# Optimization experiments

Measured on AMD Instinct MI355X. Metric: run time of the kernel, lower is better.

The kernel has to match this reference:

```python
import jax, jax.numpy as jnp
import numpy as np

HIDDEN = 64
PRED_LEN = 12
B = 32768
OBS_LEN = 20


def setup_inputs() -> dict:
    key = jax.random.key(0)
    ks = jax.random.split(key, 16)
    bound = 1.0 / np.sqrt(HIDDEN)  # PyTorch default LSTM init range
    u = lambda k, shape: jax.random.uniform(k, shape, jnp.float32, -bound, bound)
    return {
        "obs_seq": jax.random.normal(ks[0], (B, OBS_LEN, 2), jnp.float32),
        "w_ih_l0": u(ks[1], (4 * HIDDEN, 2)),
        "w_hh_l0": u(ks[2], (4 * HIDDEN, HIDDEN)),
        "b_ih_l0": u(ks[3], (4 * HIDDEN,)),
        "b_hh_l0": u(ks[4], (4 * HIDDEN,)),
        "w_ih_l1": u(ks[5], (4 * HIDDEN, HIDDEN)),
        "w_hh_l1": u(ks[6], (4 * HIDDEN, HIDDEN)),
        "b_ih_l1": u(ks[7], (4 * HIDDEN,)),
        "b_hh_l1": u(ks[8], (4 * HIDDEN,)),
        "dec_w_ih": u(ks[9], (4 * HIDDEN, 2)),
        "dec_w_hh": u(ks[10], (4 * HIDDEN, HIDDEN)),
        "dec_b_ih": u(ks[11], (4 * HIDDEN,)),
        "dec_b_hh": u(ks[12], (4 * HIDDEN,)),
        "out_w": u(ks[13], (2, HIDDEN)),
        "out_b": u(ks[14], (2,)),
    }


def _lstm_cell(x, h, c, w_ih, w_hh, b):
    # PyTorch gate order: input, forget, cell(g), output
    z = x @ w_ih.T + h @ w_hh.T + b
    i, f, g, o = jnp.split(z, 4, axis=-1)
    c_new = jax.nn.sigmoid(f) * c + jax.nn.sigmoid(i) * jnp.tanh(g)
    h_new = jax.nn.sigmoid(o) * jnp.tanh(c_new)
    return h_new, c_new


def _lstm_layer(x_tbd, w_ih, w_hh, b, h0, c0):
    # x_tbd: (T, B, in). Returns all hidden states (T, B, H) and final (h, c).
    def step(carry, x_t):
        h, c = carry
        h, c = _lstm_cell(x_t, h, c, w_ih, w_hh, b)
        return (h, c), h
    (h, c), hs = jax.lax.scan(step, (h0, c0), x_tbd)
    return hs, h, c


def reference(obs_seq, w_ih_l0, w_hh_l0, b_ih_l0, b_hh_l0,
              w_ih_l1, w_hh_l1, b_ih_l1, b_hh_l1,
              dec_w_ih, dec_w_hh, dec_b_ih, dec_b_hh, out_w, out_b):
    # Eval-mode reference: dropout layers act as identity.
    bsz = obs_seq.shape[0]
    x = jnp.transpose(obs_seq, (1, 0, 2))  # (T, B, 2)
    zeros = jnp.zeros((bsz, HIDDEN), obs_seq.dtype)
    hs1, _, _ = _lstm_layer(x, w_ih_l0, w_hh_l0, b_ih_l0 + b_hh_l0, zeros, zeros)
    _, h, c = _lstm_layer(hs1, w_ih_l1, w_hh_l1, b_ih_l1 + b_hh_l1, zeros, zeros)
    db = dec_b_ih + dec_b_hh

    def dec_step(carry, _):
        h, c, xin = carry
        h, c = _lstm_cell(xin, h, c, dec_w_ih, dec_w_hh, db)
        out = h @ out_w.T + out_b
        return (h, c, out), out

    _, preds = jax.lax.scan(dec_step, (h, c, obs_seq[:, -1, :]), None, length=PRED_LEN)
    return jnp.transpose(preds, (1, 0, 2))  # (B, pred_len, 2)
```

## Files before the change

### kernel.cpp

```cpp
#include <hip/hip_runtime.h>
#include <math.h>

#define BATCH 32768
#define TOBS  20
#define TPRED 12

typedef _Float16 f16;
typedef f16  half8 __attribute__((ext_vector_type(8)));
typedef float f32x4 __attribute__((ext_vector_type(4)));

#define LOG2E 1.44269504088896f
#define K2    2.88539008177793f

#define OFF_W0A  0u
#define OFF_WDA  36864u
#define OFF_W1   73728u
#define OFF_B1   139264u
#define OFF_OUT  140288u
#define WS_NEED  ((size_t)143360)

__device__ __forceinline__ float frcp(float x){
#if __has_builtin(__builtin_amdgcn_rcpf)
  return __builtin_amdgcn_rcpf(x);
#else
  return 1.0f/x;
#endif
}
__device__ __forceinline__ float fexp2(float x){
#if __has_builtin(__builtin_amdgcn_exp2f)
  return __builtin_amdgcn_exp2f(x);
#else
  return exp2f(x);
#endif
}
__device__ __forceinline__ f32x4 MFMA(half8 a, half8 b, f32x4 c){
  return __builtin_amdgcn_mfma_f32_16x16x32_f16(a, b, c, 0, 0, 0);
}
__device__ __forceinline__ int grow(int rt, int m){
  return (m&3)*64 + (m>>2)*16 + rt;
}
__device__ __forceinline__ float gsc(int m){
  return ((m&3)==2) ? (2.0f*LOG2E) : LOG2E;
}

__device__ __forceinline__ float gate_h(const f32x4 a, float& c){
  const float ei = fexp2(-a[0]);
  const float ef = fexp2(-a[1]);
  const float eg = fexp2(-a[2]);
  const float eo = fexp2(-a[3]);
  const float fg  = frcp(1.0f + ef);
  const float rig = frcp((1.0f + ei)*(1.0f + eg));
  const float cn  = fg*c + (1.0f - eg)*rig;
  c = cn;
  const float ec = fexp2(cn * -K2);
  return (1.0f - ec) * frcp((1.0f + eo)*(1.0f + ec));
}

__global__ void prep_pack(const float* __restrict__ wih0, const float* __restrict__ whh0,
                          const float* __restrict__ bih0, const float* __restrict__ bhh0,
                          const float* __restrict__ wih1, const float* __restrict__ whh1,
                          const float* __restrict__ bih1, const float* __restrict__ bhh1,
                          const float* __restrict__ dwih, const float* __restrict__ dwhh,
                          const float* __restrict__ dbih, const float* __restrict__ dbhh,
                          const float* __restrict__ outw, const float* __restrict__ outb,
                          char* __restrict__ ws)
{
  const int tid = blockIdx.x*blockDim.x + threadIdx.x;
  const int stride = gridDim.x*blockDim.x;

  f16* w0 = (f16*)(ws + OFF_W0A);
  f16* wd = (f16*)(ws + OFF_WDA);
  for (int idx = tid; idx < 16384; idx += stride) {
    int i = idx & 7, lane = (idx>>3)&63, kt = (idx>>9)&1, rt = idx>>10;
    int m = lane&15;
    int row = grow(rt, m);
    int k   = kt*32 + (lane>>4)*8 + i;
    float s = gsc(m);
    w0[idx] = (f16)(whh0[row*64 + k]*s);
    wd[idx] = (f16)(dwhh[row*64 + k]*s);
  }
  for (int idx = tid; idx < 2048; idx += stride) {
    int i = idx & 7, m = (idx>>3)&15, rt = idx>>7;
    int row = grow(rt, m);
    float s = gsc(m);
    float v0 = (i==0) ? wih0[row*2] : (i==1) ? wih0[row*2+1] : (i==2) ? (bih0[row]+bhh0[row]) : 0.f;
    float vd = (i==0) ? dwih[row*2] : (i==1) ? dwih[row*2+1] : (i==2) ? (dbih[row]+dbhh[row]) : 0.f;
    w0[16384 + idx] = (f16)(v0*s);
    wd[16384 + idx] = (f16)(vd*s);
  }
  f16* w1 = (f16*)(ws + OFF_W1);
  for (int idx = tid; idx < 32768; idx += stride) {
    int i = idx & 7, lane = (idx>>3)&63, kt = (idx>>9)&3, rt = idx>>11;
    int m = lane&15;
    int row = grow(rt, m);
    int k   = kt*32 + (lane>>4)*8 + i;
    float s = gsc(m);
    w1[idx] = (f16)(((k < 64) ? wih1[row*64 + k] : whh1[row*64 + (k-64)])*s);
  }
  float* b1 = (float*)(ws + OFF_B1);
  for (int idx = tid; idx < 256; idx += stride) {
    int m = idx & 15, rt = idx >> 4;
    int row = grow(rt, m);
    b1[idx] = (bih1[row] + bhh1[row])*gsc(m);
  }
  f16* wo = (f16*)(ws + OFF_OUT);
  for (int idx = tid; idx < 1536; idx += stride) {
    int i = idx & 7, lane = (idx>>3)&63, kt = idx>>9;
    int m = lane&15;
    int k = kt*32 + (lane>>4)*8 + i;
    float v = 0.f;
    if (m < 2) {
      if (k < 64) v = outw[m*64 + k];
      else if (k == 64) v = outb[m];
    }
    wo[idx] = (f16)v;
  }
}

__global__ __launch_bounds__(512, 2)
void lstm_mfma(const float* __restrict__ obs, char* __restrict__ ws, float* __restrict__ out)
{
  __shared__ __align__(16) f16   lw[18432];
  __shared__ __align__(16) f16   lw1[32768];
  __shared__ __align__(16) float lb1[256];
  __shared__ __align__(16) f16   lout[1536];
  __shared__ __align__(16) f16   h0buf[4][2][2304];
  __shared__ __align__(16) f16   s1b[4][2304];

  const int tid  = threadIdx.x;
  const int wv   = tid >> 6;
  const int lane = tid & 63;
  const int pr   = wv >> 1;
  const int role = wv & 1;
  const int n    = lane & 15;
  const int quad = lane >> 4;
  const int e0   = blockIdx.x*128 + pr*32;
  const size_t bn  = (size_t)(e0 + n);
  const size_t bn2 = (size_t)(e0 + 16 + n);

  {
    uint4* d = (uint4*)lw;
    const uint4* s = (const uint4*)(ws + OFF_W0A);
    for (int i = tid; i < 2304; i += 512) d[i] = s[i];
    uint4* d1 = (uint4*)lw1;
    const uint4* s1g = (const uint4*)(ws + OFF_W1);
    #pragma unroll
    for (int i = 0; i < 8; ++i) d1[tid + 512*i] = s1g[tid + 512*i];
    if (tid < 64)  ((uint4*)lb1)[tid] = ((const uint4*)(ws + OFF_B1))[tid];
    if (tid < 192) ((uint4*)lout)[tid] = ((const uint4*)(ws + OFF_OUT))[tid];
    uint4 z = {0,0,0,0};
    uint4* zp = (uint4*)&h0buf[0][0][0];
    for (int i = tid; i < 2304; i += 512) zp[i] = z;
    uint4* zq = (uint4*)&s1b[0][0];
    for (int i = tid; i < 1152; i += 512) zq[i] = z;
  }
  __syncthreads();

  const half8* AW  = (const half8*)lw;
  const half8* AWX = (const half8*)(lw + 16384);
  const half8* GA  = (const half8*)lw1;
  const half8* LO  = (const half8*)lout;
  f16* s1 = &s1b[pr][0];

  float ccA[16], ccB[16];
  #pragma unroll
  for (int q = 0; q < 16; ++q) { ccA[q] = 0.f; ccB[q] = 0.f; }

  const int brd  = n*72 + quad*8;
  const int brd2 = (n+16)*72 + quad*8;
  const int hwA  = n*72 + quad*16;
  const int hwB  = (n+16)*72 + quad*16;

  float2 xvA, xvB;
  if (role == 0) {
    xvA = *(const float2*)(obs + (bn *TOBS + 0)*2);
    xvB = *(const float2*)(obs + (bn2*TOBS + 0)*2);
  }

  for (int t = 0; t <= TOBS; ++t) {
    if (role == 0) {
      if (t < TOBS) {
        float2 xA1 = make_float2(0.f,0.f), xB1 = make_float2(0.f,0.f);
        if (t+1 < TOBS) {
          xA1 = *(const float2*)(obs + (bn *TOBS + t+1)*2);
          xB1 = *(const float2*)(obs + (bn2*TOBS + t+1)*2);
        }
        half8 bx  = (half8)(f16)0;
        half8 bx2 = (half8)(f16)0;
        if (quad == 0) {
          bx[0]  = (f16)xvA.x; bx[1]  = (f16)xvA.y; bx[2]  = (f16)1.0f;
          bx2[0] = (f16)xvB.x; bx2[1] = (f16)xvB.y; bx2[2] = (f16)1.0f;
        }
        const f16* rb = &h0buf[pr][(t&1)^1][0];
        f16*       wb = &h0buf[pr][(t&1)][0];
        const half8 hb0  = *(const half8*)(rb + brd);
        const half8 hb1  = *(const half8*)(rb + brd + 32);
        const half8 hb0b = *(const half8*)(rb + brd2);
        const half8 hb1b = *(const half8*)(rb + brd2 + 32);
        half8 hvA0, hvA1, hvB0, hvB1;
        #pragma unroll
        for (int rt = 0; rt < 16; ++rt) {
          const half8 wA0 = AW[(rt*2+0)*64 + lane];
          const half8 wA1 = AW[(rt*2+1)*64 + lane];
          const half8 wAX = AWX[rt*16 + n];
          f32x4 a = {0.f,0.f,0.f,0.f};
          a = MFMA(wA0, hb0, a); a = MFMA(wA1, hb1, a); a = MFMA(wAX, bx, a);
          f32x4 a2 = {0.f,0.f,0.f,0.f};
          a2 = MFMA(wA0, hb0b, a2); a2 = MFMA(wA1, hb1b, a2); a2 = MFMA(wAX, bx2, a2);
          {
            const f16 h = (f16)gate_h(a, ccA[rt]);
            if (rt < 8) hvA0[rt] = h; else hvA1[rt-8] = h;
          }
          {
            const f16 h = (f16)gate_h(a2, ccB[rt]);
            if (rt < 8) hvB0[rt] = h; else hvB1[rt-8] = h;
          }
        }
        *(half8*)(wb + hwA)     = hvA0;
        *(half8*)(wb + hwA + 8) = hvA1;
        *(half8*)(wb + hwB)     = hvB0;
        *(half8*)(wb + hwB + 8) = hvB1;
        xvA = xA1; xvB = xB1;
      }
    } else {
      if (t >= 1) {
        const f16* gb = &h0buf[pr][(t&1)^1][0];
        const half8 g0  = *(const half8*)(gb + brd);
        const half8 g1  = *(const half8*)(gb + brd + 32);
        const half8 g2  = *(const half8*)(s1 + brd);
        const half8 g3  = *(const half8*)(s1 + brd + 32);
        const half8 g0b = *(const half8*)(gb + brd2);
        const half8 g1b = *(const half8*)(gb + brd2 + 32);
        const half8 g2b = *(const half8*)(s1 + brd2);
        const half8 g3b = *(const half8*)(s1 + brd2 + 32);
        half8 hvA0, hvA1, hvB0, hvB1;
        #pragma unroll
        for (int rt = 0; rt < 16; ++rt) {
          const half8 w0_ = GA[(rt*4+0)*64 + lane];
          const half8 w1_ = GA[(rt*4+1)*64 + lane];
          const half8 w2_ = GA[(rt*4+2)*64 + lane];
          const half8 w3_ = GA[(rt*4+3)*64 + lane];
          const f32x4 bz = *(const f32x4*)(lb1 + rt*16 + quad*4);
          f32x4 a = bz;
          a = MFMA(w0_, g0, a); a = MFMA(w1_, g1, a);
          a = MFMA(w2_, g2, a); a = MFMA(w3_, g3, a);
          f32x4 a2 = bz;
          a2 = MFMA(w0_, g0b, a2); a2 = MFMA(w1_, g1b, a2);
          a2 = MFMA(w2_, g2b, a2); a2 = MFMA(w3_, g3b, a2);
          {
            const f16 h = (f16)gate_h(a, ccA[rt]);
            if (rt < 8) hvA0[rt] = h; else hvA1[rt-8] = h;
          }
          {
            const f16 h = (f16)gate_h(a2, ccB[rt]);
            if (rt < 8) hvB0[rt] = h; else hvB1[rt-8] = h;
          }
        }
        *(half8*)(s1 + hwA)     = hvA0;
        *(half8*)(s1 + hwA + 8) = hvA1;
        *(half8*)(s1 + hwB)     = hvB0;
        *(half8*)(s1 + hwB + 8) = hvB1;
      }
    }
    __syncthreads();
  }

  {
    uint4* d = (uint4*)lw;
    const uint4* s = (const uint4*)(ws + OFF_WDA);
    for (int i = tid; i < 2304; i += 512) d[i] = s[i];
    if (role == 1) {
      float* ctr = (float*)&h0buf[pr][0][0];
      #pragma unroll
      for (int q = 0; q < 4; ++q)
        *(f32x4*)(ctr + lane*16 + q*4) = *(const f32x4*)(&ccB[q*4]);
    }
  }
  __syncthreads();

  {
    float cdec[16];
    if (role == 1) {
      #pragma unroll
      for (int q = 0; q < 16; ++q) cdec[q] = ccA[q];
    } else {
      const float* ctr = (const float*)&h0buf[pr][0][0];
      #pragma unroll
      for (int q = 0; q < 4; ++q)
        *(f32x4*)(&cdec[q*4]) = *(const f32x4*)(ctr + lane*16 + q*4);
    }
    const int    brdD = role ? brd : brd2;
    const int    hwD  = role ? hwA : hwB;
    const size_t bnD  = role ? bn  : bn2;

    float x0, x1;
    {
      const float2 xd = *(const float2*)(obs + (bnD*TOBS + (TOBS-1))*2);
      x0 = xd.x; x1 = xd.y;
    }
    half8 ob1 = (half8)(f16)0;
    if (quad == 0) ob1[0] = (f16)1.0f;

    for (int p = 0; p < TPRED; ++p) {
      half8 bx = (half8)(f16)0;
      if (quad == 0) { bx[0] = (f16)x0; bx[1] = (f16)x1; bx[2] = (f16)1.0f; }

      const half8 hb0 = *(const half8*)(s1 + brdD);
      const half8 hb1 = *(const half8*)(s1 + brdD + 32);
      half8 hv0, hv1;
      #pragma unroll
      for (int rt = 0; rt < 16; ++rt) {
        f32x4 a = {0.f,0.f,0.f,0.f};
        a = MFMA(AW[(rt*2+0)*64 + lane], hb0, a);
        a = MFMA(AW[(rt*2+1)*64 + lane], hb1, a);
        a = MFMA(AWX[rt*16 + n],          bx,  a);
        const f16 h = (f16)gate_h(a, cdec[rt]);
        if (rt < 8) hv0[rt] = h; else hv1[rt-8] = h;
      }
      *(half8*)(s1 + hwD)     = hv0;
      *(half8*)(s1 + hwD + 8) = hv1;

      const half8 nh0 = *(const half8*)(s1 + brdD);
      const half8 nh1 = *(const half8*)(s1 + brdD + 32);
      f32x4 oa = {0.f,0.f,0.f,0.f};
      oa = MFMA(LO[0*64 + lane], nh0, oa);
      oa = MFMA(LO[1*64 + lane], nh1, oa);
      oa = MFMA(LO[2*64 + lane], ob1, oa);

      if (lane < 16)
        *(float2*)(out + (bnD*TPRED + p)*2) = make_float2(oa[0], oa[1]);
      x0 = __shfl(oa[0], n, 64);
      x1 = __shfl(oa[1], n, 64);
    }
  }
}

__global__ void lstm_naive(const float* __restrict__ obs,
    const float* wih0, const float* whh0, const float* bih0, const float* bhh0,
    const float* wih1, const float* whh1, const float* bih1, const float* bhh1,
    const float* dwih, const float* dwhh, const float* dbih, const float* dbhh,
    const float* outw, const float* outb, float* __restrict__ out)
{
  const int b = blockIdx.x*blockDim.x + threadIdx.x;
  if (b >= BATCH) return;
  float h0[64], c0[64], h1[64], c1[64], t0[64], t1[64];
  for (int j=0;j<64;j++){ h0[j]=0.f; c0[j]=0.f; h1[j]=0.f; c1[j]=0.f; }
  for (int t=0;t<TOBS;t++){
    const float x0 = obs[((size_t)b*TOBS+t)*2], x1 = obs[((size_t)b*TOBS+t)*2+1];
    for (int j=0;j<64;j++){
      float zz[4];
      for (int g=0;g<4;g++){
        const int r = g*64+j;
        float acc = bih0[r]+bhh0[r] + wih0[r*2]*x0 + wih0[r*2+1]*x1;
        for (int k=0;k<64;k++) acc += whh0[r*64+k]*h0[k];
        zz[g]=acc;
      }
      const float ig=1.f/(1.f+expf(-zz[0])), fg=1.f/(1.f+expf(-zz[1]));
      const float gg=tanhf(zz[2]), og=1.f/(1.f+expf(-zz[3]));
      c0[j]=fg*c0[j]+ig*gg; t0[j]=og*tanhf(c0[j]);
    }
    for (int j=0;j<64;j++){
      float zz[4];
      for (int g=0;g<4;g++){
        const int r = g*64+j;
        float acc = bih1[r]+bhh1[r];
        for (int k=0;k<64;k++) acc += wih1[r*64+k]*t0[k] + whh1[r*64+k]*h1[k];
        zz[g]=acc;
      }
      const float ig=1.f/(1.f+expf(-zz[0])), fg=1.f/(1.f+expf(-zz[1]));
      const float gg=tanhf(zz[2]), og=1.f/(1.f+expf(-zz[3]));
      c1[j]=fg*c1[j]+ig*gg; t1[j]=og*tanhf(c1[j]);
    }
    for (int j=0;j<64;j++){ h0[j]=t0[j]; h1[j]=t1[j]; }
  }
  float x0 = obs[((size_t)b*TOBS+19)*2], x1 = obs[((size_t)b*TOBS+19)*2+1];
  for (int p=0;p<TPRED;p++){
    for (int j=0;j<64;j++){
      float zz[4];
      for (int g=0;g<4;g++){
        const int r = g*64+j;
        float acc = dbih[r]+dbhh[r] + dwih[r*2]*x0 + dwih[r*2+1]*x1;
        for (int k=0;k<64;k++) acc += dwhh[r*64+k]*h1[k];
        zz[g]=acc;
      }
      const float ig=1.f/(1.f+expf(-zz[0])), fg=1.f/(1.f+expf(-zz[1]));
      const float gg=tanhf(zz[2]), og=1.f/(1.f+expf(-zz[3]));
      c1[j]=fg*c1[j]+ig*gg; t1[j]=og*tanhf(c1[j]);
    }
    for (int j=0;j<64;j++) h1[j]=t1[j];
    float o0=outb[0], o1=outb[1];
    for (int k=0;k<64;k++){ o0+=outw[k]*h1[k]; o1+=outw[64+k]*h1[k]; }
    out[((size_t)b*TPRED+p)*2]=o0; out[((size_t)b*TPRED+p)*2+1]=o1;
    x0=o0; x1=o1;
  }
}

extern "C" void kernel_launch(void* const* d_in, const int* in_sizes, int n_in,
                              void* d_out, int out_size, void* d_ws, size_t ws_size,
                              hipStream_t stream)
{
  const float* obs  = (const float*)d_in[0];
  const float* wih0 = (const float*)d_in[1];
  const float* whh0 = (const float*)d_in[2];
  const float* bih0 = (const float*)d_in[3];
  const float* bhh0 = (const float*)d_in[4];
  const float* wih1 = (const float*)d_in[5];
  const float* whh1 = (const float*)d_in[6];
  const float* bih1 = (const float*)d_in[7];
  const float* bhh1 = (const float*)d_in[8];
  const float* dwih = (const float*)d_in[9];
  const float* dwhh = (const float*)d_in[10];
  const float* dbih = (const float*)d_in[11];
  const float* dbhh = (const float*)d_in[12];
  const float* outw = (const float*)d_in[13];
  const float* outb = (const float*)d_in[14];
  float* outp = (float*)d_out;

  if (ws_size >= WS_NEED) {
    char* ws = (char*)d_ws;
    prep_pack<<<64, 256, 0, stream>>>(wih0, whh0, bih0, bhh0, wih1, whh1, bih1, bhh1,
                                      dwih, dwhh, dbih, dbhh, outw, outb, ws);
    lstm_mfma<<<256, 512, 0, stream>>>(obs, ws, outp);
  } else {
    lstm_naive<<<(BATCH+255)/256, 256, 0, stream>>>(obs, wih0, whh0, bih0, bhh0,
        wih1, whh1, bih1, bhh1, dwih, dwhh, dbih, dbhh, outw, outb, outp);
  }
}
```

Before: 224.5 us.

## Split each LSTM role across two waves by gate-row halves with 1024-thread blocks

Doubles the block to 1024 threads so that each of the layer-0 and layer-1 roles is split across two waves, each computing half of the hidden rows (8 of 16 row tiles). Hidden-state reads are hoisted before an extra barrier so both halves can write the shared buffers safely. The decoder now spreads its work over all four waves per group with ping-pong buffers and an added barrier per prediction step. This is meant to cut per-wave serial latency on the recurrent chain and halve per-thread cell-state registers, at the cost of an extra block-wide barrier per timestep. The 256-block grid now has twice the threads per block, which raises the shared-memory and occupancy pressure per CU.

```diff
diff --git a/kernel.cpp b/kernel.cpp
--- a/kernel.cpp
+++ b/kernel.cpp
@@ -117,7 +117,7 @@
   }
 }
 
-__global__ __launch_bounds__(512, 2)
+__global__ __launch_bounds__(1024, 4)
 void lstm_mfma(const float* __restrict__ obs, char* __restrict__ ws, float* __restrict__ out)
 {
   __shared__ __align__(16) f16   lw[18432];
@@ -130,29 +130,32 @@
   const int tid  = threadIdx.x;
   const int wv   = tid >> 6;
   const int lane = tid & 63;
-  const int pr   = wv >> 1;
-  const int role = wv & 1;
+  const int grp  = wv >> 2;
+  const int sub  = wv & 3;
+  const int role = sub >> 1;
+  const int rh   = sub & 1;
+  const int R    = rh*8;
   const int n    = lane & 15;
   const int quad = lane >> 4;
-  const int e0   = blockIdx.x*128 + pr*32;
+  const int e0   = blockIdx.x*128 + grp*32;
   const size_t bn  = (size_t)(e0 + n);
   const size_t bn2 = (size_t)(e0 + 16 + n);
 
   {
     uint4* d = (uint4*)lw;
     const uint4* s = (const uint4*)(ws + OFF_W0A);
-    for (int i = tid; i < 2304; i += 512) d[i] = s[i];
+    for (int i = tid; i < 2304; i += 1024) d[i] = s[i];
     uint4* d1 = (uint4*)lw1;
     const uint4* s1g = (const uint4*)(ws + OFF_W1);
     #pragma unroll
-    for (int i = 0; i < 8; ++i) d1[tid + 512*i] = s1g[tid + 512*i];
+    for (int i = 0; i < 4; ++i) d1[tid + 1024*i] = s1g[tid + 1024*i];
     if (tid < 64)  ((uint4*)lb1)[tid] = ((const uint4*)(ws + OFF_B1))[tid];
     if (tid < 192) ((uint4*)lout)[tid] = ((const uint4*)(ws + OFF_OUT))[tid];
     uint4 z = {0,0,0,0};
     uint4* zp = (uint4*)&h0buf[0][0][0];
-    for (int i = tid; i < 2304; i += 512) zp[i] = z;
+    for (int i = tid; i < 2304; i += 1024) zp[i] = z;
     uint4* zq = (uint4*)&s1b[0][0];
-    for (int i = tid; i < 1152; i += 512) zq[i] = z;
+    for (int i = tid; i < 1152; i += 1024) zq[i] = z;
   }
   __syncthreads();
 
@@ -160,16 +163,16 @@
   const half8* AWX = (const half8*)(lw + 16384);
   const half8* GA  = (const half8*)lw1;
   const half8* LO  = (const half8*)lout;
-  f16* s1 = &s1b[pr][0];
-
-  float ccA[16], ccB[16];
+  f16* s1 = &s1b[grp][0];
+
+  float ccA[8], ccB[8];
   #pragma unroll
-  for (int q = 0; q < 16; ++q) { ccA[q] = 0.f; ccB[q] = 0.f; }
+  for (int q = 0; q < 8; ++q) { ccA[q] = 0.f; ccB[q] = 0.f; }
 
   const int brd  = n*72 + quad*8;
   const int brd2 = (n+16)*72 + quad*8;
-  const int hwA  = n*72 + quad*16;
-  const int hwB  = (n+16)*72 + quad*16;
+  const int hwAw = n*72 + quad*16 + R;
+  const int hwBw = (n+16)*72 + quad*16 + R;
 
   float2 xvA, xvB;
   if (role == 0) {
@@ -178,28 +181,48 @@
   }
 
   for (int t = 0; t <= TOBS; ++t) {
+    half8 hb0, hb1, hb0b, hb1b;
+    half8 g0, g1, g2, g3, g0b, g1b, g2b, g3b;
+    half8 bx = (half8)(f16)0, bx2 = (half8)(f16)0;
+    float2 xA1, xB1;
     if (role == 0) {
       if (t < TOBS) {
-        float2 xA1 = make_float2(0.f,0.f), xB1 = make_float2(0.f,0.f);
+        xA1 = make_float2(0.f,0.f); xB1 = make_float2(0.f,0.f);
         if (t+1 < TOBS) {
           xA1 = *(const float2*)(obs + (bn *TOBS + t+1)*2);
           xB1 = *(const float2*)(obs + (bn2*TOBS + t+1)*2);
         }
-        half8 bx  = (half8)(f16)0;
-        half8 bx2 = (half8)(f16)0;
         if (quad == 0) {
           bx[0]  = (f16)xvA.x; bx[1]  = (f16)xvA.y; bx[2]  = (f16)1.0f;
           bx2[0] = (f16)xvB.x; bx2[1] = (f16)xvB.y; bx2[2] = (f16)1.0f;
         }
-        const f16* rb = &h0buf[pr][(t&1)^1][0];
-        f16*       wb = &h0buf[pr][(t&1)][0];
-        const half8 hb0  = *(const half8*)(rb + brd);
-        const half8 hb1  = *(const half8*)(rb + brd + 32);
-        const half8 hb0b = *(const half8*)(rb + brd2);
-        const half8 hb1b = *(const half8*)(rb + brd2 + 32);
-        half8 hvA0, hvA1, hvB0, hvB1;
+        const f16* rb = &h0buf[grp][(t&1)^1][0];
+        hb0  = *(const half8*)(rb + brd);
+        hb1  = *(const half8*)(rb + brd + 32);
+        hb0b = *(const half8*)(rb + brd2);
+        hb1b = *(const half8*)(rb + brd2 + 32);
+      }
+    } else {
+      if (t >= 1) {
+        const f16* gb = &h0buf[grp][(t&1)^1][0];
+        g0  = *(const half8*)(gb + brd);
+        g1  = *(const half8*)(gb + brd + 32);
+        g2  = *(const half8*)(s1 + brd);
+        g3  = *(const half8*)(s1 + brd + 32);
+        g0b = *(const half8*)(gb + brd2);
+        g1b = *(const half8*)(gb + brd2 + 32);
+        g2b = *(const half8*)(s1 + brd2);
+        g3b = *(const half8*)(s1 + brd2 + 32);
+      }
+    }
+    __syncthreads();
+    if (role == 0) {
+      if (t < TOBS) {
+        f16* wb = &h0buf[grp][(t&1)][0];
+        half8 hvA, hvB;
         #pragma unroll
-        for (int rt = 0; rt < 16; ++rt) {
+        for (int r = 0; r < 8; ++r) {
+          const int rt = R + r;
           const half8 wA0 = AW[(rt*2+0)*64 + lane];
           const half8 wA1 = AW[(rt*2+1)*64 + lane];
           const half8 wAX = AWX[rt*16 + n];
@@ -207,35 +230,19 @@
           a = MFMA(wA0, hb0, a); a = MFMA(wA1, hb1, a); a = MFMA(wAX, bx, a);
           f32x4 a2 = {0.f,0.f,0.f,0.f};
           a2 = MFMA(wA0, hb0b, a2); a2 = MFMA(wA1, hb1b, a2); a2 = MFMA(wAX, bx2, a2);
-          {
-            const f16 h = (f16)gate_h(a, ccA[rt]);
-            if (rt < 8) hvA0[rt] = h; else hvA1[rt-8] = h;
-          }
-          {
-            const f16 h = (f16)gate_h(a2, ccB[rt]);
-            if (rt < 8) hvB0[rt] = h; else hvB1[rt-8] = h;
-          }
+          hvA[r] = (f16)gate_h(a,  ccA[r]);
+          hvB[r] = (f16)gate_h(a2, ccB[r]);
         }
-        *(half8*)(wb + hwA)     = hvA0;
-        *(half8*)(wb + hwA + 8) = hvA1;
-        *(half8*)(wb + hwB)     = hvB0;
-        *(half8*)(wb + hwB + 8) = hvB1;
+        *(half8*)(wb + hwAw) = hvA;
+        *(half8*)(wb + hwBw) = hvB;
         xvA = xA1; xvB = xB1;
       }
     } else {
       if (t >= 1) {
-        const f16* gb = &h0buf[pr][(t&1)^1][0];
-        const half8 g0  = *(const half8*)(gb + brd);
-        const half8 g1  = *(const half8*)(gb + brd + 32);
-        const half8 g2  = *(const half8*)(s1 + brd);
-        const half8 g3  = *(const half8*)(s1 + brd + 32);
-        const half8 g0b = *(const half8*)(gb + brd2);
-        const half8 g1b = *(const half8*)(gb + brd2 + 32);
-        const half8 g2b = *(const half8*)(s1 + brd2);
-        const half8 g3b = *(const half8*)(s1 + brd2 + 32);
-        half8 hvA0, hvA1, hvB0, hvB1;
+        half8 hvA, hvB;
         #pragma unroll
-        for (int rt = 0; rt < 16; ++rt) {
+        for (int r = 0; r < 8; ++r) {
+          const int rt = R + r;
           const half8 w0_ = GA[(rt*4+0)*64 + lane];
           const half8 w1_ = GA[(rt*4+1)*64 + lane];
           const half8 w2_ = GA[(rt*4+2)*64 + lane];
@@ -247,19 +254,11 @@
           f32x4 a2 = bz;
           a2 = MFMA(w0_, g0b, a2); a2 = MFMA(w1_, g1b, a2);
           a2 = MFMA(w2_, g2b, a2); a2 = MFMA(w3_, g3b, a2);
-          {
-            const f16 h = (f16)gate_h(a, ccA[rt]);
-            if (rt < 8) hvA0[rt] = h; else hvA1[rt-8] = h;
-          }
-          {
-            const f16 h = (f16)gate_h(a2, ccB[rt]);
-            if (rt < 8) hvB0[rt] = h; else hvB1[rt-8] = h;
-          }
+          hvA[r] = (f16)gate_h(a,  ccA[r]);
+          hvB[r] = (f16)gate_h(a2, ccB[r]);
         }
-        *(half8*)(s1 + hwA)     = hvA0;
-        *(half8*)(s1 + hwA + 8) = hvA1;
-        *(half8*)(s1 + hwB)     = hvB0;
-        *(half8*)(s1 + hwB + 8) = hvB1;
+        *(half8*)(s1 + hwAw) = hvA;
+        *(half8*)(s1 + hwBw) = hvB;
       }
     }
     __syncthreads();
@@ -268,30 +267,33 @@
   {
     uint4* d = (uint4*)lw;
     const uint4* s = (const uint4*)(ws + OFF_WDA);
-    for (int i = tid; i < 2304; i += 512) d[i] = s[i];
+    for (int i = tid; i < 2304; i += 1024) d[i] = s[i];
     if (role == 1) {
-      float* ctr = (float*)&h0buf[pr][0][0];
+      float* ctr = (float*)&h0buf[grp][0][0];
       #pragma unroll
-      for (int q = 0; q < 4; ++q)
-        *(f32x4*)(ctr + lane*16 + q*4) = *(const f32x4*)(&ccB[q*4]);
+      for (int r = 0; r < 8; ++r) {
+        ctr[(0*16 + R + r)*64 + lane] = ccA[r];
+        ctr[(1*16 + R + r)*64 + lane] = ccB[r];
+      }
     }
   }
   __syncthreads();
 
   {
-    float cdec[16];
-    if (role == 1) {
+    const int cs  = sub >> 1;
+    const int rhD = sub & 1;
+    const int RD  = rhD*8;
+    float cdec[8];
+    {
+      const float* ctr = (const float*)&h0buf[grp][0][0];
       #pragma unroll
-      for (int q = 0; q < 16; ++q) cdec[q] = ccA[q];
-    } else {
-      const float* ctr = (const float*)&h0buf[pr][0][0];
-      #pragma unroll
-      for (int q = 0; q < 4; ++q)
-        *(f32x4*)(&cdec[q*4]) = *(const f32x4*)(ctr + lane*16 + q*4);
-    }
-    const int    brdD = role ? brd : brd2;
-    const int    hwD  = role ? hwA : hwB;
-    const size_t bnD  = role ? bn  : bn2;
+      for (int r = 0; r < 8; ++r) cdec[r] = ctr[(cs*16 + RD + r)*64 + lane];
+    }
+    __syncthreads();
+
+    const int    brdD = cs ? brd2 : brd;
+    const int    hwDw = (cs ? (n+16)*72 : n*72) + quad*16 + RD;
+    const size_t bnD  = (size_t)(e0 + cs*16 + n);
 
     float x0, x1;
     {
@@ -301,33 +303,39 @@
     half8 ob1 = (half8)(f16)0;
     if (quad == 0) ob1[0] = (f16)1.0f;
 
+    f16* buf0 = (f16*)&h0buf[grp][0][0];
+    f16* buf1 = s1;
+
     for (int p = 0; p < TPRED; ++p) {
+      f16*       wr = (p & 1) ? buf1 : buf0;
+      const f16* rd = (p & 1) ? buf0 : buf1;
+
       half8 bx = (half8)(f16)0;
       if (quad == 0) { bx[0] = (f16)x0; bx[1] = (f16)x1; bx[2] = (f16)1.0f; }
 
-      const half8 hb0 = *(const half8*)(s1 + brdD);
-      const half8 hb1 = *(const half8*)(s1 + brdD + 32);
-      half8 hv0, hv1;
+      const half8 hb0 = *(const half8*)(rd + brdD);
+      const half8 hb1 = *(const half8*)(rd + brdD + 32);
+      half8 hv;
       #pragma unroll
-      for (int rt = 0; rt < 16; ++rt) {
+      for (int r = 0; r < 8; ++r) {
+        const int rt = RD + r;
         f32x4 a = {0.f,0.f,0.f,0.f};
         a = MFMA(AW[(rt*2+0)*64 + lane], hb0, a);
         a = MFMA(AW[(rt*2+1)*64 + lane], hb1, a);
         a = MFMA(AWX[rt*16 + n],          bx,  a);
-        const f16 h = (f16)gate_h(a, cdec[rt]);
-        if (rt < 8) hv0[rt] = h; else hv1[rt-8] = h;
-      }
-      *(half8*)(s1 + hwD)     = hv0;
-      *(half8*)(s1 + hwD + 8) = hv1;
-
-      const half8 nh0 = *(const half8*)(s1 + brdD);
-      const half8 nh1 = *(const half8*)(s1 + brdD + 32);
+        hv[r] = (f16)gate_h(a, cdec[r]);
+      }
+      *(half8*)(wr + hwDw) = hv;
+      __syncthreads();
+
+      const half8 nh0 = *(const half8*)(wr + brdD);
+      const half8 nh1 = *(const half8*)(wr + brdD + 32);
       f32x4 oa = {0.f,0.f,0.f,0.f};
       oa = MFMA(LO[0*64 + lane], nh0, oa);
       oa = MFMA(LO[1*64 + lane], nh1, oa);
       oa = MFMA(LO[2*64 + lane], ob1, oa);
 
-      if (lane < 16)
+      if (lane < 16 && rhD == 0)
         *(float2*)(out + (bnD*TPRED + p)*2) = make_float2(oa[0], oa[1]);
       x0 = __shfl(oa[0], n, 64);
       x1 = __shfl(oa[1], n, 64);
@@ -420,7 +428,7 @@
     char* ws = (char*)d_ws;
     prep_pack<<<64, 256, 0, stream>>>(wih0, whh0, bih0, bhh0, wih1, whh1, bih1, bhh1,
                                       dwih, dwhh, dbih, dbhh, outw, outb, ws);
-    lstm_mfma<<<256, 512, 0, stream>>>(obs, ws, outp);
+    lstm_mfma<<<256, 1024, 0, stream>>>(obs, ws, outp);
   } else {
     lstm_naive<<<(BATCH+255)/256, 256, 0, stream>>>(obs, wih0, whh0, bih0, bhh0,
         wih1, whh1, bih1, bhh1, dwih, dwhh, dbih, dbhh, outw, outb, outp);
```

After: 302.2 us. +34.6%, slower.
